# Kernel optimization log

Measured on AMD Instinct MI355X. Metric: run time of the kernel, lower is better.

Reference implementation:

```python
import jax, jax.numpy as jnp
import numpy as np

# ---- static config (mirrors TALoss(num_classes=80, reg_max=16, strides=[8,16,32])) ----
B, M, NC, REG_MAX = 32, 20, 80, 16
STRIDES = (8, 16, 32)
HW = ((80, 80), (40, 40), (20, 20))          # feature map sizes for 640x640 input
NO = REG_MAX * 4 + NC                         # 144 channels per head
A = sum(h * w for h, w in HW)                 # 8400 anchors
TOPK, ALPHA, BETA = 10, 0.5, 6.0
BOX_G, CLS_G, DFL_G = 7.5, 0.5, 1.5
EPS = 1e-9


def setup_inputs() -> dict:
    key = jax.random.key(0)
    ks = jax.random.split(key, 6)
    feats = {f"feat{i}": jax.random.normal(ks[i], (B, NO, h, w), jnp.float32)
             for i, (h, w) in enumerate(HW)}
    # targets: (N,6) rows of (img_idx, class, cx, cy, w, h), normalized, 20 boxes/image, sorted by image
    img_idx = jnp.repeat(jnp.arange(B, dtype=jnp.float32), M)
    cls = jax.random.randint(ks[3], (B * M,), 0, NC).astype(jnp.float32)
    cxy = jax.random.uniform(ks[4], (B * M, 2), minval=0.2, maxval=0.8)
    wh = jax.random.uniform(ks[5], (B * M, 2), minval=0.05, maxval=0.3)
    targets = jnp.concatenate([img_idx[:, None], cls[:, None], cxy, wh], axis=1)
    return {**feats, "targets": targets}


def _make_anchors():
    pts, strs = [], []
    for (h, w), s in zip(HW, STRIDES):
        sx = jnp.arange(w, dtype=jnp.float32) + 0.5
        sy = jnp.arange(h, dtype=jnp.float32) + 0.5
        gy, gx = jnp.meshgrid(sy, sx, indexing="ij")
        pts.append(jnp.stack([gx, gy], -1).reshape(-1, 2))
        strs.append(jnp.full((h * w, 1), float(s), jnp.float32))
    return jnp.concatenate(pts), jnp.concatenate(strs)   # (A,2), (A,1)


def _ciou(b1, b2, eps=1e-7):
    # b1, b2: broadcastable xyxy boxes (..., 4) -> CIoU (...,)
    b1x1, b1y1, b1x2, b1y2 = b1[..., 0], b1[..., 1], b1[..., 2], b1[..., 3]
    b2x1, b2y1, b2x2, b2y2 = b2[..., 0], b2[..., 1], b2[..., 2], b2[..., 3]
    w1, h1 = b1x2 - b1x1, b1y2 - b1y1 + eps
    w2, h2 = b2x2 - b2x1, b2y2 - b2y1 + eps
    inter = (jnp.clip(jnp.minimum(b1x2, b2x2) - jnp.maximum(b1x1, b2x1), 0)
             * jnp.clip(jnp.minimum(b1y2, b2y2) - jnp.maximum(b1y1, b2y1), 0))
    union = w1 * h1 + w2 * h2 - inter + eps
    iou = inter / union
    cw = jnp.maximum(b1x2, b2x2) - jnp.minimum(b1x1, b2x1)
    ch = jnp.maximum(b1y2, b2y2) - jnp.minimum(b1y1, b2y1)
    c2 = cw ** 2 + ch ** 2 + eps
    rho2 = ((b2x1 + b2x2 - b1x1 - b1x2) ** 2 + (b2y1 + b2y2 - b1y1 - b1y2) ** 2) / 4.0
    v = (4.0 / np.pi ** 2) * (jnp.arctan(w2 / h2) - jnp.arctan(w1 / h1)) ** 2
    a = jax.lax.stop_gradient(v / (v - iou + (1.0 + eps)))   # torch: computed under no_grad
    return iou - (rho2 / c2 + v * a)


def _assign(pd_scores, pd_bboxes, anc, gt_labels, gt_bboxes, mask_gt):
    """TaskAlignedAssigner. pd_scores (B,A,NC) sigmoid-ed, pd_bboxes (B,A,4) image units,
    anc (A,2) image units, gt_labels (B,M), gt_bboxes (B,M,4), mask_gt (B,M) float."""
    # anchors inside each gt box -> (B,M,A)
    lt = anc[None, None, :, :] - gt_bboxes[:, :, None, :2]
    rb = gt_bboxes[:, :, None, 2:] - anc[None, None, :, :]
    mask_in = (jnp.concatenate([lt, rb], -1).min(-1) > EPS).astype(jnp.float32)
    mask = mask_in * mask_gt[..., None]                      # (B,M,A) candidate mask
    overlaps = jnp.clip(_ciou(gt_bboxes[:, :, None, :], pd_bboxes[:, None, :, :]), 0) * mask
    labels = gt_labels.astype(jnp.int32)                     # (B,M)
    # scores of each gt's class at every anchor: (B,M,A)
    bbox_scores = jnp.take_along_axis(pd_scores.transpose(0, 2, 1),
                                      jnp.broadcast_to(labels[:, :, None], (B, M, A)), axis=1) * mask
    align = (bbox_scores ** ALPHA) * (overlaps ** BETA)      # (B,M,A), already zero off-mask
    # top-k anchors per gt
    _, idxs = jax.lax.top_k(align, TOPK)                     # (B,M,K)
    idxs = jnp.where(mask_gt[..., None] > 0, idxs, 0)
    cnt = jax.nn.one_hot(idxs, A, dtype=jnp.float32).sum(-2)  # (B,M,A)
    mask_topk = jnp.where(cnt > 1, 0.0, cnt)
    mask_pos = mask_topk * mask
    # resolve anchors matched to multiple gts: keep the max-overlap gt
    fg = mask_pos.sum(1)                                     # (B,A)
    is_max = jnp.moveaxis(jax.nn.one_hot(overlaps.argmax(1), M, dtype=jnp.float32), -1, 1)  # (B,M,A)
    mask_pos = jnp.where(fg[:, None, :] > 1, is_max, mask_pos)
    fg = mask_pos.sum(1)
    tgt_idx = mask_pos.argmax(1)                             # (B,A)
    t_labels = jnp.take_along_axis(labels, tgt_idx, 1)       # (B,A)
    t_bboxes = jnp.take_along_axis(gt_bboxes, tgt_idx[..., None], 1)  # (B,A,4)
    fg_b = (fg > 0).astype(jnp.float32)
    t_scores = jax.nn.one_hot(t_labels, NC, dtype=jnp.float32) * fg_b[..., None]
    # normalize scores: align * (max overlap per gt) / (max align per gt)
    align_pos = align * mask_pos
    pos_align = align_pos.max(-1, keepdims=True)             # (B,M,1)
    pos_over = (overlaps * mask_pos).max(-1, keepdims=True)
    norm = (align_pos * pos_over / (pos_align + EPS)).max(1)  # (B,A)
    return t_bboxes, t_scores * norm[..., None], fg_b


def _forward(feat0, feat1, feat2, targets):
    feats = [feat0, feat1, feat2]
    pred = jnp.concatenate([f.reshape(B, NO, -1) for f in feats], axis=2)
    pred_distri = pred[:, :REG_MAX * 4].transpose(0, 2, 1)   # (B,A,64)
    pred_scores = pred[:, REG_MAX * 4:].transpose(0, 2, 1)   # (B,A,NC)
    anc, stride_t = _make_anchors()
    img_h, img_w = HW[0][0] * STRIDES[0], HW[0][1] * STRIDES[0]
    scale = jnp.array([img_w, img_h, img_w, img_h], jnp.float32)
    # ---- preprocess targets (N,6) -> padded (B,M,5), xywh*scale -> xyxy ----
    idx = targets[:, 0].astype(jnp.int32)
    pos = jnp.arange(targets.shape[0]) - jnp.searchsorted(idx, idx, side="left")
    out = jnp.zeros((B, M, 5), jnp.float32).at[idx, pos].set(targets[:, 1:])
    gt_labels = out[..., 0]
    xywh = out[..., 1:5] * scale
    gt_bboxes = jnp.concatenate([xywh[..., :2] - xywh[..., 2:] / 2,
                                 xywh[..., :2] + xywh[..., 2:] / 2], -1)
    mask_gt = (gt_bboxes.sum(-1) > 0).astype(jnp.float32)    # (B,M)
    # ---- DFL bbox decode (feature-map units) ----
    proj = jnp.arange(REG_MAX, dtype=jnp.float32)
    dist = jax.nn.softmax(pred_distri.reshape(B, A, 4, REG_MAX), -1) @ proj  # (B,A,4) ltrb
    pred_bboxes = jnp.concatenate([anc - dist[..., :2], anc + dist[..., 2:]], -1)
    # ---- task-aligned assignment (on detached preds, image units) ----
    pd_scores = jax.lax.stop_gradient(jax.nn.sigmoid(pred_scores))
    pd_bboxes = jax.lax.stop_gradient(pred_bboxes) * stride_t
    target_bboxes, target_scores, fg_mask = _assign(pd_scores, pd_bboxes, anc * stride_t,
                                                    gt_labels, gt_bboxes, mask_gt)
    target_bboxes = target_bboxes / stride_t
    tss = jnp.maximum(target_scores.sum(), 1.0)
    # ---- BCE-with-logits classification loss (pos_weight=1) ----
    x, t = pred_scores, target_scores
    bce = jnp.maximum(x, 0) - x * t + jnp.log1p(jnp.exp(-jnp.abs(x)))
    loss_cls = bce.sum() / tss
    # ---- CIoU box loss + DFL, weighted by per-anchor target score sum on fg ----
    weight = target_scores.sum(-1) * fg_mask                 # (B,A)
    iou = _ciou(pred_bboxes, target_bboxes)
    loss_box = ((1.0 - iou) * weight).sum() / tss
    tltrb = jnp.clip(jnp.concatenate([anc - target_bboxes[..., :2],
                                      target_bboxes[..., 2:] - anc], -1),
                     0, REG_MAX - 1 - 0.01)                  # (B,A,4)
    logp = jax.nn.log_softmax(pred_distri.reshape(B, A, 4, REG_MAX), -1)
    tl = tltrb.astype(jnp.int32)
    wl = (tl + 1).astype(jnp.float32) - tltrb
    nll_l = -jnp.take_along_axis(logp, tl[..., None], -1)[..., 0]
    nll_r = -jnp.take_along_axis(logp, (tl + 1)[..., None], -1)[..., 0]
    dfl = (nll_l * wl + nll_r * (1.0 - wl)).mean(-1)         # (B,A)
    loss_dfl = (dfl * weight).sum() / tss
    losses = jnp.stack([loss_box * BOX_G, loss_cls * CLS_G, loss_dfl * DFL_G])
    return losses.sum() * B, jax.lax.stop_gradient(losses)


def reference(feat0, feat1, feat2, targets):
    return _forward(feat0, feat1, feat2, targets)
```

## Files before the change

### kernel.cpp

```cpp
#include <hip/hip_runtime.h>
#include <math.h>

constexpr int BB  = 32;
constexpr int MM  = 20;
constexpr int NCC = 80;
constexpr int RM  = 16;
constexpr int NOC = 144;
constexpr int AT  = 8400;
constexpr int TK  = 10;
constexpr int BA  = BB * AT;
constexpr int BM  = BB * MM;
constexpr int MAXPOS = BM * TK;
constexpr int NSLOT = 1024;
constexpr float EPS_A = 1e-9f;
constexpr float VCOEF = 0.40528473456935108577551785283891f;

constexpr int NT0 = BB * 6400 / 256;
constexpr int NT1 = BB * 1600 / 256;
constexpr int NT2 = BB * 400 / 256;
constexpr int NTT = NT0 + NT1 + NT2;

struct Lvl { const float* f; int o, w, hw; float s; };

__device__ inline Lvl level_of(int a, const float* f0, const float* f1, const float* f2){
  Lvl L;
  if (a < 6400)      { L.f = f0; L.o = a;        L.w = 80; L.hw = 6400; L.s = 8.f;  }
  else if (a < 8000) { L.f = f1; L.o = a - 6400; L.w = 40; L.hw = 1600; L.s = 16.f; }
  else               { L.f = f2; L.o = a - 8000; L.w = 20; L.hw = 400;  L.s = 32.f; }
  return L;
}

__device__ inline float frcp(float x){ return __builtin_amdgcn_rcpf(x); }

__device__ inline float fast_atan(float x){
  float ax = fabsf(x);
  bool big = ax > 1.f;
  float z = big ? frcp(ax) : ax;
  float z2 = z * z;
  float p = fmaf(z2, -0.0117212f, 0.0526533f);
  p = fmaf(z2, p, -0.1164329f);
  p = fmaf(z2, p, 0.1935435f);
  p = fmaf(z2, p, -0.3326235f);
  p = fmaf(z2, p, 0.9999773f);
  float r = z * p;
  r = big ? 1.57079632679f - r : r;
  return copysignf(r, x);
}

__device__ inline float ciou_f(float b1x1,float b1y1,float b1x2,float b1y2,
                               float b2x1,float b2y1,float b2x2,float b2y2){
  const float eps = 1e-7f;
  float w1 = b1x2 - b1x1, h1 = b1y2 - b1y1 + eps;
  float w2 = b2x2 - b2x1, h2 = b2y2 - b2y1 + eps;
  float iw = fmaxf(fminf(b1x2, b2x2) - fmaxf(b1x1, b2x1), 0.f);
  float ih = fmaxf(fminf(b1y2, b2y2) - fmaxf(b1y1, b2y1), 0.f);
  float inter = iw * ih;
  float uni = w1 * h1 + w2 * h2 - inter + eps;
  float iou = inter * frcp(uni);
  float cw = fmaxf(b1x2, b2x2) - fminf(b1x1, b2x1);
  float ch = fmaxf(b1y2, b2y2) - fminf(b1y1, b2y1);
  float c2 = cw * cw + ch * ch + eps;
  float dx = b2x1 + b2x2 - b1x1 - b1x2;
  float dy = b2y1 + b2y2 - b1y1 - b1y2;
  float rho2 = (dx * dx + dy * dy) * 0.25f;
  float r1 = w1 * frcp(h1), r2 = w2 * frcp(h2);
  float dat = fast_atan((r2 - r1) * frcp(fmaf(r1, r2, 1.f)));
  float v = VCOEF * dat * dat;
  float alpha = v * frcp(v - iou + (1.0f + eps));
  return iou - (rho2 * frcp(c2) + v * alpha);
}

__device__ inline unsigned long long shfl_xor_u64(unsigned long long v, int mask){
  int lo = __shfl_xor((int)(unsigned)(v & 0xFFFFFFFFull), mask);
  int hi = __shfl_xor((int)(unsigned)(v >> 32), mask);
  return ((unsigned long long)(unsigned)hi << 32) | (unsigned)lo;
}

__device__ inline float softplus4(float4 v){
  float s = fmaxf(v.x, 0.f) + __logf(1.f + __expf(-fabsf(v.x)));
  s += fmaxf(v.y, 0.f) + __logf(1.f + __expf(-fabsf(v.y)));
  s += fmaxf(v.z, 0.f) + __logf(1.f + __expf(-fabsf(v.z)));
  s += fmaxf(v.w, 0.f) + __logf(1.f + __expf(-fabsf(v.w)));
  return s;
}

template<int HW, int W, int AOFF>
__device__ inline float fused_side(const float* __restrict__ f, int t,
                                   float* __restrict__ pbox_f,
                                   float* __restrict__ lse_f,
                                   unsigned* __restrict__ mpos){
  constexpr int HW4 = HW / 4;
  int lq = t >> 2, s = t & 3;
  int b = lq / HW4, o4 = lq - b * HW4;
  int o = o4 * 4;
  const float* base = f + (size_t)b * NOC * HW + o;

  float4 x[16];
#pragma unroll
  for (int j = 0; j < 16; j++)
    x[j] = *(const float4*)(base + (size_t)((s * 16 + j) * HW));
  float mx0 = x[0].x, mx1 = x[0].y, mx2 = x[0].z, mx3 = x[0].w;
#pragma unroll
  for (int j = 1; j < 16; j++){
    mx0 = fmaxf(mx0, x[j].x); mx1 = fmaxf(mx1, x[j].y);
    mx2 = fmaxf(mx2, x[j].z); mx3 = fmaxf(mx3, x[j].w);
  }
  float sm0 = 0.f, sm1 = 0.f, sm2 = 0.f, sm3 = 0.f;
  float dt0 = 0.f, dt1 = 0.f, dt2 = 0.f, dt3 = 0.f;
#pragma unroll
  for (int j = 0; j < 16; j++){
    float e0 = __expf(x[j].x - mx0), e1 = __expf(x[j].y - mx1);
    float e2 = __expf(x[j].z - mx2), e3 = __expf(x[j].w - mx3);
    sm0 += e0; sm1 += e1; sm2 += e2; sm3 += e3;
    dt0 = fmaf(e0, (float)j, dt0); dt1 = fmaf(e1, (float)j, dt1);
    dt2 = fmaf(e2, (float)j, dt2); dt3 = fmaf(e3, (float)j, dt3);
  }
  float d[4]  = { dt0 * frcp(sm0), dt1 * frcp(sm1), dt2 * frcp(sm2), dt3 * frcp(sm3) };
  float ls[4] = { mx0 + __logf(sm0), mx1 + __logf(sm1),
                  mx2 + __logf(sm2), mx3 + __logf(sm3) };

  int gi0 = b * AT + AOFF + o;
#pragma unroll
  for (int k = 0; k < 4; k++){
    int ok = o + k;
    int iy = ok / W;
    float ax = (float)(ok - iy * W) + 0.5f;
    float ay = (float)iy + 0.5f;
    float coord = (s == 0 || s == 2) ? ax : ay;
    float v = (s < 2) ? (coord - d[k]) : (coord + d[k]);
    pbox_f[(size_t)(gi0 + k) * 4 + s] = v;
    lse_f [(size_t)(gi0 + k) * 4 + s] = ls[k];
  }
  if (s == 0) *(uint4*)(&mpos[gi0]) = make_uint4(0u, 0u, 0u, 0u);

  const float* cbase = base + (size_t)((4 * RM) + s * 20) * HW;
  float sp = 0.f;
#pragma unroll
  for (int jj = 0; jj < 20; jj += 10){
    float4 xx[10];
#pragma unroll
    for (int j = 0; j < 10; j++)
      xx[j] = *(const float4*)(cbase + (size_t)((jj + j) * HW));
#pragma unroll
    for (int j = 0; j < 10; j++)
      sp += softplus4(xx[j]);
  }
  return sp;
}

__global__ __launch_bounds__(256) void k_feat5(
    const float* __restrict__ f0, const float* __restrict__ f1,
    const float* __restrict__ f2, const float* __restrict__ tgt,
    float* __restrict__ pbox_f, float* __restrict__ lse_f,
    unsigned* __restrict__ mpos, double* __restrict__ bce_part,
    float* __restrict__ out5, float* __restrict__ gtbox,
    int* __restrict__ gtlab, float* __restrict__ gtmask,
    int* __restrict__ pa_i, int* __restrict__ po_i,
    int* __restrict__ topk_arr, double* __restrict__ acc){
  __shared__ float red[4];
  int blk = blockIdx.x;
  int tid = threadIdx.x;
  if (blk < NTT){
    float sp;
    if (blk < NT0){
      sp = fused_side<6400, 80, 0>(f0, blk * 256 + tid, pbox_f, lse_f, mpos);
    } else if (blk < NT0 + NT1){
      sp = fused_side<1600, 40, 6400>(f1, (blk - NT0) * 256 + tid, pbox_f, lse_f, mpos);
    } else {
      sp = fused_side<400, 20, 8000>(f2, (blk - NT0 - NT1) * 256 + tid, pbox_f, lse_f, mpos);
    }
    for (int off = 32; off; off >>= 1) sp += __shfl_down(sp, off);
    int wid = tid >> 6, lid = tid & 63;
    if (lid == 0) red[wid] = sp;
    __syncthreads();
    if (tid == 0) bce_part[blk] = (double)(red[0] + red[1] + red[2] + red[3]);
  } else {
    for (int i = tid; i < BM * 5; i += 256) out5[i] = 0.f;
    for (int i = tid; i < MAXPOS; i += 256) topk_arr[i] = -1;
    for (int i = tid; i < BM; i += 256){ pa_i[i] = 0; po_i[i] = 0; }
    if (tid < 8) acc[tid] = 0.0;
    __syncthreads();
    for (int t = tid; t < BM; t += 256){
      int img = (int)tgt[t * 6 + 0];
      int j = t;
      while (j > 0 && (int)tgt[(j - 1) * 6 + 0] == img) j--;
      int pos = t - j;
      if (img >= 0 && img < BB && pos < MM){
        for (int k = 0; k < 5; k++)
          out5[(img * MM + pos) * 5 + k] = tgt[t * 6 + 1 + k];
      }
    }
    __syncthreads();
    for (int t = tid; t < BM; t += 256){
      float lab = out5[t * 5 + 0];
      float cx = out5[t * 5 + 1] * 640.f;
      float cy = out5[t * 5 + 2] * 640.f;
      float w  = out5[t * 5 + 3] * 640.f;
      float h  = out5[t * 5 + 4] * 640.f;
      float x1 = cx - w * 0.5f, y1 = cy - h * 0.5f;
      float x2 = cx + w * 0.5f, y2 = cy + h * 0.5f;
      gtbox[t * 4 + 0] = x1; gtbox[t * 4 + 1] = y1;
      gtbox[t * 4 + 2] = x2; gtbox[t * 4 + 3] = y2;
      gtlab[t] = (int)lab;
      gtmask[t] = ((x1 + y1 + x2 + y2) > 0.f) ? 1.f : 0.f;
    }
  }
}

__global__ __launch_bounds__(256) void k_align(
    const float* __restrict__ f0, const float* __restrict__ f1,
    const float* __restrict__ f2, const float4* __restrict__ pbox,
    const float* __restrict__ gtbox, const int* __restrict__ gtlab,
    const float* __restrict__ gtmask,
    unsigned* __restrict__ mpos, int* __restrict__ topk_arr){
  int pair = blockIdx.x;
  int b = pair / MM, m = pair % MM;
  if (gtmask[pair] <= 0.f) return;
  int tid = threadIdx.x;
  float gx1 = gtbox[pair * 4 + 0], gy1 = gtbox[pair * 4 + 1];
  float gx2 = gtbox[pair * 4 + 2], gy2 = gtbox[pair * 4 + 3];
  int lab = gtlab[pair];
  __shared__ float s_val[NSLOT];
  __shared__ int   s_anc[NSLOT];
  __shared__ unsigned long long s_red[4];
  __shared__ int   s_win[TK];
  int base = 0;

#define PROC_LEVEL(FPTR, W, HW, AOFF, S)                                      \
  {                                                                           \
    const float s_ = (S); const float inv_ = 1.f / (S);                       \
    int x0 = max(0, (int)floorf(gx1 * inv_ - 0.5f));                          \
    int x1 = min((W) - 1, (int)ceilf(gx2 * inv_ - 0.5f));                     \
    int y0 = max(0, (int)floorf(gy1 * inv_ - 0.5f));                          \
    int y1 = min((W) - 1, (int)ceilf(gy2 * inv_ - 0.5f));                     \
    int nxx = x1 - x0 + 1, nyy = y1 - y0 + 1;                                 \
    if (nxx > 0 && nyy > 0){                                                  \
      int ntot = nxx * nyy;                                                   \
      unsigned magic = 0xFFFFFFFFu / (unsigned)nxx + 1u;                      \
      const float* clsrow = (FPTR) + (size_t)b * NOC * (HW)                   \
                            + (size_t)(4 * RM + lab) * (HW);                  \
      for (int t = tid; t < ntot; t += 256){                                  \
        int slot = base + t;                                                  \
        if (slot >= NSLOT) break;                                             \
        int iy = (int)(((unsigned long long)(unsigned)t * magic) >> 32);      \
        int ix = t - iy * nxx + x0;                                           \
        iy += y0;                                                             \
        float ax = ((float)ix + 0.5f) * s_;                                   \
        float ay = ((float)iy + 0.5f) * s_;                                   \
        float mn = fminf(fminf(ax - gx1, ay - gy1),                           \
                         fminf(gx2 - ax, gy2 - ay));                          \
        int o = iy * (W) + ix;                                                \
        int a = (AOFF) + o;                                                   \
        float aln = -1.f;                                                     \
        if (mn > EPS_A){                                                      \
          float4 pb = pbox[b * AT + a];                                       \
          float c = ciou_f(gx1, gy1, gx2, gy2,                                \
                           pb.x * s_, pb.y * s_, pb.z * s_, pb.w * s_);       \
          float ovl = fmaxf(c, 0.f);                                          \
          if (ovl > 0.f){                                                     \
            float xv = clsrow[o];                                             \
            float sc = frcp(1.f + __expf(-xv));                               \
            float o2 = ovl * ovl;                                             \
            aln = sqrtf(sc) * (o2 * o2 * o2);                                 \
          }                                                                   \
        }                                                                     \
        s_val[slot] = aln;                                                    \
        s_anc[slot] = a;                                                      \
      }                                                                       \
      base += ntot;                                                           \
    }                                                                         \
  }

  PROC_LEVEL(f0, 80, 6400, 0, 8.f)
  PROC_LEVEL(f1, 40, 1600, 6400, 16.f)
  PROC_LEVEL(f2, 20, 400, 8000, 32.f)
#undef PROC_LEVEL

  __syncthreads();
  int total = min(base, NSLOT);
  int wid = tid >> 6, lid = tid & 63;
  for (int r = 0; r < TK; r++){
    unsigned long long key = 0ULL;
    for (int i = tid; i < total; i += 256){
      float v = s_val[i];
      if (v > 0.f){
        unsigned long long k2 =
            ((unsigned long long)__float_as_uint(v) << 32) |
            (unsigned long long)(0xFFFFFFFFu - (unsigned)i);
        key = key > k2 ? key : k2;
      }
    }
    for (int xm = 1; xm < 64; xm <<= 1){
      unsigned long long o = shfl_xor_u64(key, xm);
      key = key > o ? key : o;
    }
    if (lid == 0) s_red[wid] = key;
    __syncthreads();
    if (tid == 0){
      unsigned long long k = s_red[0];
      k = k > s_red[1] ? k : s_red[1];
      k = k > s_red[2] ? k : s_red[2];
      k = k > s_red[3] ? k : s_red[3];
      if (k){
        int slot = (int)(0xFFFFFFFFu - (unsigned)(k & 0xFFFFFFFFull));
        s_win[r] = s_anc[slot];
        s_val[slot] = -1.f;
      } else s_win[r] = -1;
    }
    __syncthreads();
  }
  if (tid < TK){
    int a = s_win[tid];
    topk_arr[pair * TK + tid] = a;
    if (a >= 0) atomicOr(&mpos[(size_t)b * AT + a], 1u << m);
  }
}

__global__ __launch_bounds__(256) void k_resolve(
    const float* __restrict__ f0, const float* __restrict__ f1,
    const float* __restrict__ f2, const float4* __restrict__ pbox,
    const float* __restrict__ gtbox, const int* __restrict__ gtlab,
    const float* __restrict__ gtmask, const unsigned* __restrict__ mpos,
    const int* __restrict__ topk_arr,
    unsigned char* __restrict__ resm, float* __restrict__ resaln,
    int* __restrict__ pa_i, int* __restrict__ po_i){
  int i = blockIdx.x * 256 + threadIdx.x;
  int a = topk_arr[i];
  if (a < 0) return;
  int pair = i / TK;
  int b = pair / MM, m = pair % MM;
  unsigned bits = mpos[(size_t)b * AT + a];
  if (m != __ffs(bits) - 1) return;
  Lvl L = level_of(a, f0, f1, f2);
  float ax = ((float)(L.o % L.w) + 0.5f) * L.s;
  float ay = ((float)(L.o / L.w) + 0.5f) * L.s;
  float4 pb = pbox[b * AT + a];
  float px1 = pb.x * L.s, py1 = pb.y * L.s, px2 = pb.z * L.s, py2 = pb.w * L.s;
  int mr; float ovl;
  if (__popc(bits) > 1){
    float best = -1.f; int bm = 0;
    for (int mm = 0; mm < MM; mm++){
      float v = 0.f;
      if (gtmask[b * MM + mm] > 0.f){
        float x1 = gtbox[(b * MM + mm) * 4 + 0], y1 = gtbox[(b * MM + mm) * 4 + 1];
        float x2 = gtbox[(b * MM + mm) * 4 + 2], y2 = gtbox[(b * MM + mm) * 4 + 3];
        float mn = fminf(fminf(ax - x1, ay - y1), fminf(x2 - ax, y2 - ay));
        if (mn > EPS_A)
          v = fmaxf(ciou_f(x1, y1, x2, y2, px1, py1, px2, py2), 0.f);
      }
      if (v > best){ best = v; bm = mm; }
    }
    mr = bm; ovl = fmaxf(best, 0.f);
  } else {
    mr = m;
    float x1 = gtbox[(b * MM + mr) * 4 + 0], y1 = gtbox[(b * MM + mr) * 4 + 1];
    float x2 = gtbox[(b * MM + mr) * 4 + 2], y2 = gtbox[(b * MM + mr) * 4 + 3];
    ovl = fmaxf(ciou_f(x1, y1, x2, y2, px1, py1, px2, py2), 0.f);
  }
  int lab = gtlab[b * MM + mr];
  float xv = L.f[(size_t)b * NOC * L.hw + (size_t)(4 * RM + lab) * L.hw + L.o];
  float sc = frcp(1.f + __expf(-xv));
  float o2 = ovl * ovl;
  float aln = sqrtf(sc) * (o2 * o2 * o2);
  size_t gi = (size_t)b * AT + a;
  resm[gi] = (unsigned char)mr;
  resaln[gi] = aln;
  atomicMax(&pa_i[b * MM + mr], __float_as_int(aln));
  atomicMax(&po_i[b * MM + mr], __float_as_int(ovl));
}

__global__ __launch_bounds__(256) void k_final(
    const float* __restrict__ f0, const float* __restrict__ f1,
    const float* __restrict__ f2,
    const float4* __restrict__ pbox, const float4* __restrict__ lse,
    const float* __restrict__ gtbox, const int* __restrict__ gtlab,
    const int* __restrict__ pa_i, const int* __restrict__ po_i,
    const unsigned* __restrict__ mpos, const int* __restrict__ topk_arr,
    const unsigned char* __restrict__ resm, const float* __restrict__ resaln,
    double* __restrict__ acc){
  int i = blockIdx.x * 256 + threadIdx.x;
  float w_ = 0.f, clsp = 0.f, boxp = 0.f, dflp = 0.f;
  int a = topk_arr[i];
  if (a >= 0){
    int pair = i / TK;
    int b = pair / MM, m = pair % MM;
    unsigned bits = mpos[(size_t)b * AT + a];
    if (m == __ffs(bits) - 1){
      size_t gi = (size_t)b * AT + a;
      int mr = (int)resm[gi];
      float aln = resaln[gi];
      float pa = __int_as_float(pa_i[b * MM + mr]);
      float po = __int_as_float(po_i[b * MM + mr]);
      w_ = aln * po * frcp(pa + EPS_A);
      Lvl L = level_of(a, f0, f1, f2);
      const float* base = L.f + (size_t)b * NOC * L.hw + L.o;
      float ax = (float)(L.o % L.w) + 0.5f;
      float ay = (float)(L.o / L.w) + 0.5f;
      float inv_s = frcp(L.s);
      float tx1 = gtbox[(b * MM + mr) * 4 + 0] * inv_s, ty1 = gtbox[(b * MM + mr) * 4 + 1] * inv_s;
      float tx2 = gtbox[(b * MM + mr) * 4 + 2] * inv_s, ty2 = gtbox[(b * MM + mr) * 4 + 3] * inv_s;
      float4 pb = pbox[b * AT + a];
      float iou = ciou_f(pb.x, pb.y, pb.z, pb.w, tx1, ty1, tx2, ty2);
      boxp = (1.f - iou) * w_;
      float4 L4 = lse[b * AT + a];
      float lsv[4] = { L4.x, L4.y, L4.z, L4.w };
      float tv[4] = { ax - tx1, ay - ty1, tx2 - ax, ty2 - ay };
      float dfl = 0.f;
#pragma unroll
      for (int s4 = 0; s4 < 4; s4++){
        float t = fminf(fmaxf(tv[s4], 0.f), (float)(RM - 1) - 0.01f);
        int tl = (int)t;
        float wl = (float)(tl + 1) - t;
        float xl = base[(size_t)(s4 * RM + tl) * L.hw];
        float xr = base[(size_t)(s4 * RM + tl + 1) * L.hw];
        dfl += (lsv[s4] - xl) * wl + (lsv[s4] - xr) * (1.f - wl);
      }
      dflp = dfl * 0.25f * w_;
      int lab = gtlab[b * MM + mr];
      clsp = base[(size_t)(4 * RM + lab) * L.hw] * w_;
    }
  }
  __shared__ float red[4][4];
  float vals[4] = { w_, clsp, boxp, dflp };
  int wid = threadIdx.x >> 6, lid = threadIdx.x & 63;
#pragma unroll
  for (int j = 0; j < 4; j++){
    float v = vals[j];
    for (int off = 32; off; off >>= 1) v += __shfl_down(v, off);
    if (lid == 0) red[wid][j] = v;
  }
  __syncthreads();
  if (threadIdx.x == 0){
    float t0 = 0.f, t1 = 0.f, t2 = 0.f, t3 = 0.f;
    for (int w2 = 0; w2 < 4; w2++){
      t0 += red[w2][0]; t1 += red[w2][1]; t2 += red[w2][2]; t3 += red[w2][3];
    }
    atomicAdd(&acc[0], (double)t0);
    atomicAdd(&acc[1], (double)t1);
    atomicAdd(&acc[2], (double)t2);
    atomicAdd(&acc[3], (double)t3);
  }
}

__global__ void k_out(const double* __restrict__ acc,
                      const double* __restrict__ bce_part,
                      float* __restrict__ out){
  __shared__ double sd[256];
  double s = 0.0;
  for (int i = threadIdx.x; i < NTT; i += 256) s += bce_part[i];
  sd[threadIdx.x] = s;
  __syncthreads();
  for (int off = 128; off; off >>= 1){
    if (threadIdx.x < off) sd[threadIdx.x] += sd[threadIdx.x + off];
    __syncthreads();
  }
  if (threadIdx.x == 0){
    double bce_sum = sd[0];
    double tss = acc[0] > 1.0 ? acc[0] : 1.0;
    double loss_box = acc[2] / tss;
    double loss_cls = (bce_sum - acc[1]) / tss;
    double loss_dfl = acc[3] / tss;
    float l0 = (float)(loss_box * 7.5);
    float l1 = (float)(loss_cls * 0.5);
    float l2 = (float)(loss_dfl * 1.5);
    out[0] = (l0 + l1 + l2) * 32.f;
    out[1] = l0;
    out[2] = l1;
    out[3] = l2;
  }
}

extern "C" void kernel_launch(void* const* d_in, const int* in_sizes, int n_in,
                              void* d_out, int out_size, void* d_ws, size_t ws_size,
                              hipStream_t stream) {
  const float* f0 = (const float*)d_in[0];
  const float* f1 = (const float*)d_in[1];
  const float* f2 = (const float*)d_in[2];
  const float* tg = (const float*)d_in[3];
  float* out = (float*)d_out;

  char* w = (char*)d_ws;
  size_t off = 0;
  auto alloc = [&](size_t bytes) -> void* {
    void* p = w + off;
    off += (bytes + 255) & ~(size_t)255;
    return p;
  };
  float4*        pbox    = (float4*)       alloc((size_t)BA * 16);
  float4*        lse     = (float4*)       alloc((size_t)BA * 16);
  float*         gtbox   = (float*)        alloc((size_t)BM * 16);
  int*           gtlab   = (int*)          alloc((size_t)BM * 4);
  float*         gtmask  = (float*)        alloc((size_t)BM * 4);
  float*         out5    = (float*)        alloc((size_t)BM * 20);
  unsigned*      mpos    = (unsigned*)     alloc((size_t)BA * 4);
  int*           topk_arr= (int*)          alloc((size_t)MAXPOS * 4);
  unsigned char* resm    = (unsigned char*)alloc((size_t)BA);
  float*         resaln  = (float*)        alloc((size_t)BA * 4);
  int*           pa      = (int*)          alloc((size_t)BM * 4);
  int*           po      = (int*)          alloc((size_t)BM * 4);
  double*        acc     = (double*)       alloc(8 * 8);
  double*        bcep    = (double*)       alloc((size_t)NTT * 8);

  k_feat5<<<NTT + 1, 256, 0, stream>>>(f0, f1, f2, tg, (float*)pbox, (float*)lse,
                                       mpos, bcep, out5, gtbox, gtlab, gtmask,
                                       pa, po, topk_arr, acc);
  k_align<<<BM, 256, 0, stream>>>(f0, f1, f2, pbox, gtbox, gtlab, gtmask, mpos, topk_arr);
  k_resolve<<<MAXPOS / 256, 256, 0, stream>>>(f0, f1, f2, pbox, gtbox, gtlab, gtmask,
                                              mpos, topk_arr, resm, resaln, pa, po);
  k_final<<<MAXPOS / 256, 256, 0, stream>>>(f0, f1, f2, pbox, lse, gtbox, gtlab,
                                            pa, po, mpos, topk_arr, resm, resaln, acc);
  k_out<<<1, 256, 0, stream>>>(acc, bcep, out);
}
```

Before: 249.0 us.

## Split BCE softplus reduction out of feature kernel into grid-stride kernel

The fused feature kernel used to compute the DFL softmax, the decoded boxes and the class softplus sum in one pass. It is now split in two. k_dfl handles only the regression channels and has a launch_bounds occupancy hint. A new k_bce reads the class channels with contiguous float4 grid-stride loops over a fixed 1024 blocks. This is meant to cut register pressure and raise occupancy and coalescing, at the cost of an extra kernel launch and serialising two memory-bound passes.

```diff
diff --git a/kernel.cpp b/kernel.cpp
--- a/kernel.cpp
+++ b/kernel.cpp
@@ -19,6 +19,8 @@
 constexpr int NT1 = BB * 1600 / 256;
 constexpr int NT2 = BB * 400 / 256;
 constexpr int NTT = NT0 + NT1 + NT2;
+
+constexpr int NBCE_BLK = 1024;
 
 struct Lvl { const float* f; int o, w, hw; float s; };
 
@@ -85,10 +87,10 @@
 }
 
 template<int HW, int W, int AOFF>
-__device__ inline float fused_side(const float* __restrict__ f, int t,
-                                   float* __restrict__ pbox_f,
-                                   float* __restrict__ lse_f,
-                                   unsigned* __restrict__ mpos){
+__device__ inline void dfl_side(const float* __restrict__ f, int t,
+                                float* __restrict__ pbox_f,
+                                float* __restrict__ lse_f,
+                                unsigned* __restrict__ mpos){
   constexpr int HW4 = HW / 4;
   int lq = t >> 2, s = t & 3;
   int b = lq / HW4, o4 = lq - b * HW4;
@@ -132,48 +134,25 @@
     lse_f [(size_t)(gi0 + k) * 4 + s] = ls[k];
   }
   if (s == 0) *(uint4*)(&mpos[gi0]) = make_uint4(0u, 0u, 0u, 0u);
-
-  const float* cbase = base + (size_t)((4 * RM) + s * 20) * HW;
-  float sp = 0.f;
-#pragma unroll
-  for (int jj = 0; jj < 20; jj += 10){
-    float4 xx[10];
-#pragma unroll
-    for (int j = 0; j < 10; j++)
-      xx[j] = *(const float4*)(cbase + (size_t)((jj + j) * HW));
-#pragma unroll
-    for (int j = 0; j < 10; j++)
-      sp += softplus4(xx[j]);
-  }
-  return sp;
-}
-
-__global__ __launch_bounds__(256) void k_feat5(
+}
+
+__global__ __launch_bounds__(256, 2) void k_dfl(
     const float* __restrict__ f0, const float* __restrict__ f1,
     const float* __restrict__ f2, const float* __restrict__ tgt,
     float* __restrict__ pbox_f, float* __restrict__ lse_f,
-    unsigned* __restrict__ mpos, double* __restrict__ bce_part,
+    unsigned* __restrict__ mpos,
     float* __restrict__ out5, float* __restrict__ gtbox,
     int* __restrict__ gtlab, float* __restrict__ gtmask,
     int* __restrict__ pa_i, int* __restrict__ po_i,
     int* __restrict__ topk_arr, double* __restrict__ acc){
-  __shared__ float red[4];
   int blk = blockIdx.x;
   int tid = threadIdx.x;
-  if (blk < NTT){
-    float sp;
-    if (blk < NT0){
-      sp = fused_side<6400, 80, 0>(f0, blk * 256 + tid, pbox_f, lse_f, mpos);
-    } else if (blk < NT0 + NT1){
-      sp = fused_side<1600, 40, 6400>(f1, (blk - NT0) * 256 + tid, pbox_f, lse_f, mpos);
-    } else {
-      sp = fused_side<400, 20, 8000>(f2, (blk - NT0 - NT1) * 256 + tid, pbox_f, lse_f, mpos);
-    }
-    for (int off = 32; off; off >>= 1) sp += __shfl_down(sp, off);
-    int wid = tid >> 6, lid = tid & 63;
-    if (lid == 0) red[wid] = sp;
-    __syncthreads();
-    if (tid == 0) bce_part[blk] = (double)(red[0] + red[1] + red[2] + red[3]);
+  if (blk < NT0){
+    dfl_side<6400, 80, 0>(f0, blk * 256 + tid, pbox_f, lse_f, mpos);
+  } else if (blk < NT0 + NT1){
+    dfl_side<1600, 40, 6400>(f1, (blk - NT0) * 256 + tid, pbox_f, lse_f, mpos);
+  } else if (blk < NTT){
+    dfl_side<400, 20, 8000>(f2, (blk - NT0 - NT1) * 256 + tid, pbox_f, lse_f, mpos);
   } else {
     for (int i = tid; i < BM * 5; i += 256) out5[i] = 0.f;
     for (int i = tid; i < MAXPOS; i += 256) topk_arr[i] = -1;
@@ -205,6 +184,47 @@
       gtmask[t] = ((x1 + y1 + x2 + y2) > 0.f) ? 1.f : 0.f;
     }
   }
+}
+
+__global__ __launch_bounds__(256) void k_bce(
+    const float* __restrict__ f0, const float* __restrict__ f1,
+    const float* __restrict__ f2, double* __restrict__ bce_part){
+  float sp = 0.f;
+  unsigned g0 = blockIdx.x * 256u + threadIdx.x;
+  {
+    constexpr unsigned NPI = 80u * 6400u / 4u;
+    constexpr unsigned TOT = (unsigned)BB * NPI;
+    for (unsigned i = g0; i < TOT; i += (unsigned)NBCE_BLK * 256u){
+      unsigned b = i / NPI, r = i - b * NPI;
+      const float4* p = (const float4*)(f0 + (size_t)b * NOC * 6400 + (size_t)64 * 6400) + r;
+      sp += softplus4(*p);
+    }
+  }
+  {
+    constexpr unsigned NPI = 80u * 1600u / 4u;
+    constexpr unsigned TOT = (unsigned)BB * NPI;
+    for (unsigned i = g0; i < TOT; i += (unsigned)NBCE_BLK * 256u){
+      unsigned b = i / NPI, r = i - b * NPI;
+      const float4* p = (const float4*)(f1 + (size_t)b * NOC * 1600 + (size_t)64 * 1600) + r;
+      sp += softplus4(*p);
+    }
+  }
+  {
+    constexpr unsigned NPI = 80u * 400u / 4u;
+    constexpr unsigned TOT = (unsigned)BB * NPI;
+    for (unsigned i = g0; i < TOT; i += (unsigned)NBCE_BLK * 256u){
+      unsigned b = i / NPI, r = i - b * NPI;
+      const float4* p = (const float4*)(f2 + (size_t)b * NOC * 400 + (size_t)64 * 400) + r;
+      sp += softplus4(*p);
+    }
+  }
+  __shared__ float red[4];
+  for (int off = 32; off; off >>= 1) sp += __shfl_down(sp, off);
+  int wid = threadIdx.x >> 6, lid = threadIdx.x & 63;
+  if (lid == 0) red[wid] = sp;
+  __syncthreads();
+  if (threadIdx.x == 0)
+    bce_part[blockIdx.x] = (double)(red[0] + red[1] + red[2] + red[3]);
 }
 
 __global__ __launch_bounds__(256) void k_align(
@@ -447,7 +467,7 @@
                       float* __restrict__ out){
   __shared__ double sd[256];
   double s = 0.0;
-  for (int i = threadIdx.x; i < NTT; i += 256) s += bce_part[i];
+  for (int i = threadIdx.x; i < NBCE_BLK; i += 256) s += bce_part[i];
   sd[threadIdx.x] = s;
   __syncthreads();
   for (int off = 128; off; off >>= 1){
@@ -499,11 +519,12 @@
   int*           pa      = (int*)          alloc((size_t)BM * 4);
   int*           po      = (int*)          alloc((size_t)BM * 4);
   double*        acc     = (double*)       alloc(8 * 8);
-  double*        bcep    = (double*)       alloc((size_t)NTT * 8);
-
-  k_feat5<<<NTT + 1, 256, 0, stream>>>(f0, f1, f2, tg, (float*)pbox, (float*)lse,
-                                       mpos, bcep, out5, gtbox, gtlab, gtmask,
-                                       pa, po, topk_arr, acc);
+  double*        bcep    = (double*)       alloc((size_t)NBCE_BLK * 8);
+
+  k_dfl<<<NTT + 1, 256, 0, stream>>>(f0, f1, f2, tg, (float*)pbox, (float*)lse,
+                                     mpos, out5, gtbox, gtlab, gtmask,
+                                     pa, po, topk_arr, acc);
+  k_bce<<<NBCE_BLK, 256, 0, stream>>>(f0, f1, f2, bcep);
   k_align<<<BM, 256, 0, stream>>>(f0, f1, f2, pbox, gtbox, gtlab, gtmask, mpos, topk_arr);
   k_resolve<<<MAXPOS / 256, 256, 0, stream>>>(f0, f1, f2, pbox, gtbox, gtlab, gtmask,
                                               mpos, topk_arr, resm, resaln, pa, po);
```

Result: no change. 249.8 us (+0.3%).
